# Kernel optimization log

Hardware: AMD Instinct MI355X
Metric: run time of the kernel (lower is better)

The kernel has to match this reference:

```python
import math
import jax, jax.numpy as jnp
import numpy as np

N_HEADS = 16
NUM_BUCKETS = 32
MAX_DISTANCE = 128
ROTARY_BASE = 10000.0


def rotate_half(x):
    x1, x2 = jnp.split(x, 2, axis=-1)
    return jnp.concatenate((-x2, x1), axis=-1)


def rotary_freqs(T, dim):
    inv_freq = 1.0 / (ROTARY_BASE ** (jnp.arange(0, dim, 2, dtype=jnp.float32) / dim))
    t = jnp.arange(T, dtype=jnp.float32)
    freqs = jnp.einsum('i,j->ij', t, inv_freq)  # [T, dim/2]
    return jnp.concatenate((freqs, freqs), axis=-1)  # [T, dim]


def rel_pos_bucket_causal(rel_pos, num_buckets=NUM_BUCKETS, max_distance=MAX_DISTANCE):
    n = jnp.maximum(-rel_pos, 0)  # [T, T] int
    max_exact = num_buckets // 2
    is_small = n < max_exact
    n_safe = jnp.maximum(n, 1).astype(jnp.float32)
    val_if_large = max_exact + (
        jnp.log(n_safe / max_exact) / math.log(max_distance / max_exact) * (num_buckets - max_exact)
    ).astype(jnp.int32)
    val_if_large = jnp.minimum(val_if_large, num_buckets - 1)
    return jnp.where(is_small, n, val_if_large)


def setup_inputs() -> dict:
    key = jax.random.key(0)
    ks = jax.random.split(key, 10)
    B, T, C = 2, 2048, 1024
    s = 0.02
    return {
        'x':  jax.random.normal(ks[0], (B, T, C), dtype=jnp.float32),
        'Wq': jax.random.normal(ks[1], (C, C), dtype=jnp.float32) * s,
        'bq': jnp.zeros((C,), dtype=jnp.float32),
        'Wk': jax.random.normal(ks[2], (C, C), dtype=jnp.float32) * s,
        'bk': jnp.zeros((C,), dtype=jnp.float32),
        'Wv': jax.random.normal(ks[3], (C, C), dtype=jnp.float32) * s,
        'bv': jnp.zeros((C,), dtype=jnp.float32),
        'Wp': jax.random.normal(ks[4], (C, C), dtype=jnp.float32) * s,
        'bp': jnp.zeros((C,), dtype=jnp.float32),
        'rel_bias_table': jax.random.normal(ks[5], (NUM_BUCKETS, N_HEADS), dtype=jnp.float32) * s,
    }


def reference(x, Wq, bq, Wk, bk, Wv, bv, Wp, bp, rel_bias_table):
    B, T, C = x.shape
    H = N_HEADS
    D = C // H

    def heads(y):
        return y.reshape(B, T, H, D).transpose(0, 2, 1, 3)  # [B,H,T,D]

    q = heads(x @ Wq + bq)
    k = heads(x @ Wk + bk)
    v = heads(x @ Wv + bv)

    # rotary (use_xpos=False -> scale=1)
    freqs = rotary_freqs(T, D)  # [T, D]
    cos, sin = jnp.cos(freqs), jnp.sin(freqs)
    q = q * cos + rotate_half(q) * sin
    k = k * cos + rotate_half(k) * sin

    # relative position bias (causal, scale=1.0)
    pos = jnp.arange(T)
    rel_pos = pos[None, :] - pos[:, None]  # k_pos - q_pos
    bucket = rel_pos_bucket_causal(rel_pos)  # [T, T]
    bias = rel_bias_table[bucket]  # [T, T, H]
    bias = bias.transpose(2, 0, 1)  # [H, T, T]

    att = jnp.einsum('bhid,bhjd->bhij', q, k) + bias[None]
    att = att * (1.0 / math.sqrt(D))
    causal = pos[None, :] <= pos[:, None]  # tril mask [T, T]
    att = jnp.where(causal[None, None], att, -jnp.inf)
    att = jax.nn.softmax(att, axis=-1)

    y = jnp.einsum('bhij,bhjd->bhid', att, v)  # [B,H,T,D]
    y = y.transpose(0, 2, 1, 3).reshape(B, T, C)
    return y @ Wp + bp
```

## Files before the change

### kernel.cpp

```cpp
#include <hip/hip_runtime.h>
#include <hip/hip_bf16.h>
#include <math.h>

#define B_ 2
#define T_ 2048
#define C_ 1024
#define H_ 16
#define D_ 64
#define M_ (B_ * T_)
#define K_ 1024

#define SCALE2 0.18033688011112043f

typedef short bf16x8 __attribute__((ext_vector_type(8)));
typedef float f32x4  __attribute__((ext_vector_type(4)));
typedef unsigned int u32;

__device__ __forceinline__ float u2f(unsigned short u) {
    union { unsigned int i; float f; } v; v.i = ((unsigned int)u) << 16; return v.f;
}
__device__ __forceinline__ unsigned short f2b(float f) {
    __hip_bfloat16 h = __float2bfloat16(f);
    return *reinterpret_cast<unsigned short*>(&h);
}
__device__ __forceinline__ u32 pack_bf16_rnd(float a, float b) {
    const u32 au = __float_as_uint(a) + 0x8000u;
    const u32 bu = __float_as_uint(b) + 0x8000u;
    return __builtin_amdgcn_perm(bu, au, 0x07060302u);
}
__device__ __forceinline__ void load_lds16(const void* g, void* l) {
    __builtin_amdgcn_global_load_lds(
        (const __attribute__((address_space(1))) u32*)g,
        (__attribute__((address_space(3))) u32*)l, 16, 0, 0);
}

__global__ __launch_bounds__(256) void prep(
    const float* __restrict__ x,
    const float* __restrict__ W0, const float* __restrict__ W1,
    const float* __restrict__ W2, const float* __restrict__ W3,
    const float* __restrict__ tbl,
    unsigned short* __restrict__ xb,
    unsigned short* __restrict__ T0, unsigned short* __restrict__ T1,
    unsigned short* __restrict__ T2, unsigned short* __restrict__ T3,
    float* __restrict__ dtab, float2* __restrict__ trig)
{
    __shared__ __align__(16) unsigned short tile[64][72];
    const int bx = blockIdx.x;
    const int tid = threadIdx.x;

    if (bx < 2048) {
        const int idx = bx * 256 + tid;
        const float4 a = reinterpret_cast<const float4*>(x)[idx * 2];
        const float4 b = reinterpret_cast<const float4*>(x)[idx * 2 + 1];
        unsigned short t[8] = {f2b(a.x), f2b(a.y), f2b(a.z), f2b(a.w),
                               f2b(b.x), f2b(b.y), f2b(b.z), f2b(b.w)};
        reinterpret_cast<bf16x8*>(xb)[idx] = *reinterpret_cast<const bf16x8*>(t);
    } else if (bx < 3072) {
        const int w = bx - 2048;
        const int z = w >> 8;
        const int rem = w & 255;
        const int k0 = (rem & 15) * 64, n0 = (rem >> 4) * 64;
        const float* W = z == 0 ? W0 : z == 1 ? W1 : z == 2 ? W2 : W3;
        unsigned short* Wt = z == 0 ? T0 : z == 1 ? T1 : z == 2 ? T2 : T3;

        #pragma unroll
        for (int it = 0; it < 4; ++it) {
            const int idx = it * 256 + tid;
            const int r = idx >> 4, c = (idx & 15) * 4;
            const float4 w4 = *reinterpret_cast<const float4*>(W + (size_t)(k0 + r) * C_ + n0 + c);
            tile[r][c + 0] = f2b(w4.x); tile[r][c + 1] = f2b(w4.y);
            tile[r][c + 2] = f2b(w4.z); tile[r][c + 3] = f2b(w4.w);
        }
        __syncthreads();
        #pragma unroll
        for (int it = 0; it < 2; ++it) {
            const int idx = it * 256 + tid;
            const int nc = idx >> 3, kc = (idx & 7) * 8;
            unsigned short tmp[8];
            #pragma unroll
            for (int e = 0; e < 8; ++e) tmp[e] = tile[kc + e][nc];
            *reinterpret_cast<bf16x8*>(Wt + (size_t)(n0 + nc) * K_ + k0 + kc) =
                *reinterpret_cast<const bf16x8*>(tmp);
        }
    } else {
        const int idx = (bx - 3072) * 256 + tid;
        if (idx < H_ * T_) {
            const int h = idx >> 11, n = idx & (T_ - 1);
            int bucket;
            if (n < 16) bucket = n;
            else {
                int vb = 16 + (int)(log2f((float)n * 0.0625f) * (16.0f / 3.0f));
                bucket = vb < 31 ? vb : 31;
            }
            dtab[idx] = tbl[bucket * H_ + h] * SCALE2;
        }
        const int t = idx >> 5, j = idx & 31;
        const float inv = exp2f(-(float)j * (13.287712379549449f / 32.0f));
        const float ang = (float)t * inv;
        trig[idx] = make_float2(cosf(ang), sinf(ang));
    }
}

__device__ __forceinline__ void gemm_core(
    const unsigned short* __restrict__ A, const unsigned short* __restrict__ Bt,
    const float* __restrict__ bias, const float2* __restrict__ trig,
    float rot_scale, float* __restrict__ outf,
    unsigned short* __restrict__ outb, int mode)
{
    __shared__ __align__(16) unsigned short As[128 * 32];
    __shared__ __align__(16) unsigned short Bs[128 * 32];

    const int tid = threadIdx.x;
    const int wid = tid >> 6, lane = tid & 63;
    const int l16 = lane & 15, quad = lane >> 4;
    const int wm = wid >> 1, wn = wid & 1;
    const int m0 = blockIdx.y * 128, n0 = blockIdx.x * 128;

    f32x4 acc[4][4];
    #pragma unroll
    for (int i = 0; i < 4; ++i)
        #pragma unroll
        for (int j = 0; j < 4; ++j) acc[i][j] = (f32x4){0.f, 0.f, 0.f, 0.f};

    char* AsB = (char*)As;
    char* BsB = (char*)Bs;

    for (int k0 = 0; k0 < K_; k0 += 32) {
        __syncthreads();
        #pragma unroll
        for (int it = 0; it < 2; ++it) {
            const int idx = it * 256 + tid;
            const int row = idx >> 2, ch = (idx & 3) * 8;
            const int ldso = it * 4096 + wid * 1024;
            load_lds16(A + (size_t)(m0 + row) * K_ + k0 + ch, AsB + ldso);
            load_lds16(Bt + (size_t)(n0 + row) * K_ + k0 + ch, BsB + ldso);
        }
        __syncthreads();

        bf16x8 af[4], bf[4];
        #pragma unroll
        for (int i = 0; i < 4; ++i) {
            af[i] = *reinterpret_cast<const bf16x8*>(&As[(wm * 64 + i * 16 + l16) * 32 + quad * 8]);
            bf[i] = *reinterpret_cast<const bf16x8*>(&Bs[(wn * 64 + i * 16 + l16) * 32 + quad * 8]);
        }
        #pragma unroll
        for (int i = 0; i < 4; ++i)
            #pragma unroll
            for (int j = 0; j < 4; ++j)
                acc[i][j] = __builtin_amdgcn_mfma_f32_16x16x32_bf16(af[i], bf[j], acc[i][j], 0, 0, 0);
    }

    if (mode == 1) {
        #pragma unroll
        for (int i = 0; i < 4; ++i) {
            const int mb = m0 + wm * 64 + i * 16 + quad * 4;
            const int bb = mb >> 11, tb = mb & (T_ - 1);
            #pragma unroll
            for (int jc = 0; jc < 2; ++jc) {
                const int n_lo = n0 + wn * 64 + jc * 16 + l16;
                const int h = n_lo >> 6, d = n_lo & 63;
                const float bv_lo = bias[n_lo], bv_hi = bias[n_lo + 32];
                unsigned short* po = outb + (((size_t)bb * H_ + h) * T_ + tb) * D_ + d;
                #pragma unroll
                for (int r = 0; r < 4; ++r) {
                    const float2 cs = trig[(tb + r) * 32 + d];
                    const float a = acc[i][jc][r] + bv_lo;
                    const float b = acc[i][jc + 2][r] + bv_hi;
                    po[(size_t)r * D_]      = f2b((a * cs.x - b * cs.y) * rot_scale);
                    po[(size_t)r * D_ + 32] = f2b((b * cs.x + a * cs.y) * rot_scale);
                }
            }
        }
        return;
    }

    #pragma unroll
    for (int i = 0; i < 4; ++i) {
        const int mb = m0 + wm * 64 + i * 16 + quad * 4;
        #pragma unroll
        for (int j = 0; j < 4; ++j) {
            const int n = n0 + wn * 64 + j * 16 + l16;
            const float bv = bias[n];
            if (mode == 2) {
                const int bb = mb >> 11, t = mb & (T_ - 1);
                const int h = n >> 6, d = n & 63;
                uint2 w;
                w.x = pack_bf16_rnd(acc[i][j][0] + bv, acc[i][j][1] + bv);
                w.y = pack_bf16_rnd(acc[i][j][2] + bv, acc[i][j][3] + bv);
                *reinterpret_cast<uint2*>(
                    outb + (((size_t)bb * H_ + h) * D_ + d) * T_ + t) = w;
            } else {
                #pragma unroll
                for (int r = 0; r < 4; ++r)
                    outf[(size_t)(mb + r) * C_ + n] = acc[i][j][r] + bv;
            }
        }
    }
}

__global__ __launch_bounds__(256) void gemm_qkv(
    const unsigned short* __restrict__ A,
    const unsigned short* __restrict__ Wq, const unsigned short* __restrict__ Wk,
    const unsigned short* __restrict__ Wv,
    const float* __restrict__ bq, const float* __restrict__ bk,
    const float* __restrict__ bv, const float2* __restrict__ trig,
    unsigned short* __restrict__ Qo, unsigned short* __restrict__ Ko,
    unsigned short* __restrict__ Vto)
{
    const int z = blockIdx.z;
    const unsigned short* Bt = z == 0 ? Wq : z == 1 ? Wk : Wv;
    const float* bias = z == 0 ? bq : z == 1 ? bk : bv;
    unsigned short* outb = z == 0 ? Qo : z == 1 ? Ko : Vto;
    const float rs = z == 0 ? SCALE2 : 1.0f;
    gemm_core(A, Bt, bias, trig, rs, nullptr, outb, z == 2 ? 2 : 1);
}

__global__ __launch_bounds__(256) void gemm_proj(
    const unsigned short* __restrict__ A, const unsigned short* __restrict__ Bt,
    const float* __restrict__ bias, float* __restrict__ outf)
{
    gemm_core(A, Bt, bias, nullptr, 1.0f, outf, nullptr, 0);
}

__global__ __launch_bounds__(256) void flash_attn(
    const unsigned short* __restrict__ Q, const unsigned short* __restrict__ K,
    const unsigned short* __restrict__ Vt, const float* __restrict__ dtab,
    unsigned short* __restrict__ Y)
{
    __shared__ __align__(16) unsigned short Ks[2][64][72];
    __shared__ __align__(16) unsigned short Vs[2][64][72];
    __shared__ __align__(16) unsigned short Ps[4][16][72];
    __shared__ __align__(16) float bias_ls[64 + T_];

    const int lin = (int)(blockIdx.y * gridDim.x + blockIdx.x);
    const int bh  = lin & 31;
    const int rem = lin >> 5;
    const int h = bh & (H_ - 1), b = bh >> 4;
    const int tid = threadIdx.x;
    const int wid = tid >> 6, lane = tid & 63;
    const int l16 = lane & 15, quad = lane >> 4;
    const size_t base = (size_t)bh * T_ * D_;
    const size_t vbase = (size_t)bh * D_ * T_;

    const int qta = (rem + bh) & 15;
    const int qtb = 31 - qta;

    if (tid < 64) bias_ls[tid] = -INFINITY;
    for (int ii = tid; ii < qtb * 64 + 64; ii += 256) bias_ls[64 + ii] = dtab[h * T_ + ii];

    bf16x8 ones;
    #pragma unroll
    for (int e = 0; e < 8; ++e) ones[e] = (short)0x3F80;

    const int sr0 = tid >> 3,         sch0 = (tid & 7) * 8;
    const int sr1 = (tid + 256) >> 3, sch1 = ((tid + 256) & 7) * 8;

    bf16x8 kr[2], vr[2];
    kr[0] = *reinterpret_cast<const bf16x8*>(K + base + (size_t)sr0 * D_ + sch0);
    kr[1] = *reinterpret_cast<const bf16x8*>(K + base + (size_t)sr1 * D_ + sch1);
    vr[0] = *reinterpret_cast<const bf16x8*>(Vt + vbase + (size_t)sr0 * T_ + sch0);
    vr[1] = *reinterpret_cast<const bf16x8*>(Vt + vbase + (size_t)sr1 * T_ + sch1);
    *reinterpret_cast<bf16x8*>(&Ks[0][sr0][sch0]) = kr[0];
    *reinterpret_cast<bf16x8*>(&Ks[0][sr1][sch1]) = kr[1];
    *reinterpret_cast<bf16x8*>(&Vs[0][sr0][sch0]) = vr[0];
    *reinterpret_cast<bf16x8*>(&Vs[0][sr1][sch1]) = vr[1];
    kr[0] = *reinterpret_cast<const bf16x8*>(K + base + (size_t)(64 + sr0) * D_ + sch0);
    kr[1] = *reinterpret_cast<const bf16x8*>(K + base + (size_t)(64 + sr1) * D_ + sch1);
    vr[0] = *reinterpret_cast<const bf16x8*>(Vt + vbase + (size_t)sr0 * T_ + 64 + sch0);
    vr[1] = *reinterpret_cast<const bf16x8*>(Vt + vbase + (size_t)sr1 * T_ + 64 + sch1);
    __syncthreads();

    int t = 0;
    for (int qi = 0; qi < 2; ++qi) {
        const int qt = qi ? qta : qtb;
        const int q0 = qt * 64;
        const int arow = q0 + wid * 16 + l16;
        const int crow = q0 + wid * 16 + quad * 4;
        const int nbase = crow - l16 * 4;

        bf16x8 qf[2];
        qf[0] = *reinterpret_cast<const bf16x8*>(Q + base + (size_t)arow * D_ + quad * 8);
        qf[1] = *reinterpret_cast<const bf16x8*>(Q + base + (size_t)arow * D_ + 32 + quad * 8);

        f32x4 o[4], ol;
        #pragma unroll
        for (int c = 0; c < 4; ++c) o[c] = (f32x4){0.f, 0.f, 0.f, 0.f};
        ol = (f32x4){0.f, 0.f, 0.f, 0.f};

        for (int kt = 0; kt <= qt; ++kt, ++t) {
            const int j0 = kt * 64;
            const int cur = t & 1, nxt = cur ^ 1;

            if (t < 32) {
                *reinterpret_cast<bf16x8*>(&Ks[nxt][sr0][sch0]) = kr[0];
                *reinterpret_cast<bf16x8*>(&Ks[nxt][sr1][sch1]) = kr[1];
                *reinterpret_cast<bf16x8*>(&Vs[nxt][sr0][sch0]) = vr[0];
                *reinterpret_cast<bf16x8*>(&Vs[nxt][sr1][sch1]) = vr[1];
            }
            if (t < 31) {
                const int tn = t + 2;
                const int jn = (tn <= qtb ? tn : tn - qtb - 1) * 64;
                kr[0] = *reinterpret_cast<const bf16x8*>(K + base + (size_t)(jn + sr0) * D_ + sch0);
                kr[1] = *reinterpret_cast<const bf16x8*>(K + base + (size_t)(jn + sr1) * D_ + sch1);
                vr[0] = *reinterpret_cast<const bf16x8*>(Vt + vbase + (size_t)sr0 * T_ + jn + sch0);
                vr[1] = *reinterpret_cast<const bf16x8*>(Vt + vbase + (size_t)sr1 * T_ + jn + sch1);
            }

            const int d0 = nbase - j0;
            const f32x4 blo = *reinterpret_cast<const f32x4*>(&bias_ls[60 + d0]);
            const f32x4 bhi = *reinterpret_cast<const f32x4*>(&bias_ls[64 + d0]);

            f32x4 sc[4];
            #pragma unroll
            for (int c = 0; c < 4; ++c) {
                #pragma unroll
                for (int r = 0; r < 4; ++r)
                    sc[c][r] = (r >= c) ? bhi[r - c] : blo[4 + r - c];
            }
            __builtin_amdgcn_s_setprio(1);
            #pragma unroll
            for (int c = 0; c < 4; ++c) {
                #pragma unroll
                for (int s = 0; s < 2; ++s) {
                    bf16x8 kf = *reinterpret_cast<const bf16x8*>(
                        &Ks[cur][l16 * 4 + c][s * 32 + quad * 8]);
                    sc[c] = __builtin_amdgcn_mfma_f32_16x16x32_bf16(qf[s], kf, sc[c], 0, 0, 0);
                }
            }
            __builtin_amdgcn_s_setprio(0);

            #pragma unroll
            for (int r = 0; r < 4; ++r) {
                const float p0 = __builtin_amdgcn_exp2f(sc[0][r]);
                const float p1 = __builtin_amdgcn_exp2f(sc[1][r]);
                const float p2 = __builtin_amdgcn_exp2f(sc[2][r]);
                const float p3 = __builtin_amdgcn_exp2f(sc[3][r]);
                uint2 w;
                w.x = pack_bf16_rnd(p0, p1);
                w.y = pack_bf16_rnd(p2, p3);
                *reinterpret_cast<uint2*>(&Ps[wid][quad * 4 + r][l16 * 4]) = w;
            }

            __builtin_amdgcn_s_setprio(1);
            #pragma unroll
            for (int s = 0; s < 2; ++s) {
                bf16x8 pf = *reinterpret_cast<const bf16x8*>(&Ps[wid][l16][s * 32 + quad * 8]);
                #pragma unroll
                for (int c = 0; c < 4; ++c) {
                    bf16x8 vf = *reinterpret_cast<const bf16x8*>(&Vs[cur][c * 16 + l16][s * 32 + quad * 8]);
                    o[c] = __builtin_amdgcn_mfma_f32_16x16x32_bf16(pf, vf, o[c], 0, 0, 0);
                }
                ol = __builtin_amdgcn_mfma_f32_16x16x32_bf16(pf, ones, ol, 0, 0, 0);
            }
            __builtin_amdgcn_s_setprio(0);

            __syncthreads();
        }

        #pragma unroll
        for (int r = 0; r < 4; ++r) {
            const int i = crow + r;
            const float invl = 1.0f / ol[r];
            #pragma unroll
            for (int c = 0; c < 4; ++c)
                Y[((size_t)b * T_ + i) * C_ + h * D_ + c * 16 + l16] = f2b(o[c][r] * invl);
        }
    }
}

extern "C" void kernel_launch(void* const* d_in, const int* in_sizes, int n_in,
                              void* d_out, int out_size, void* d_ws, size_t ws_size,
                              hipStream_t stream)
{
    const float* x   = (const float*)d_in[0];
    const float* Wq  = (const float*)d_in[1];
    const float* bq  = (const float*)d_in[2];
    const float* Wk  = (const float*)d_in[3];
    const float* bk  = (const float*)d_in[4];
    const float* Wv  = (const float*)d_in[5];
    const float* bv  = (const float*)d_in[6];
    const float* Wp  = (const float*)d_in[7];
    const float* bp  = (const float*)d_in[8];
    const float* tbl = (const float*)d_in[9];
    float* out = (float*)d_out;

    const size_t n1 = (size_t)B_ * H_ * T_ * D_;
    const size_t nW = (size_t)C_ * C_;
    unsigned short* xb  = (unsigned short*)d_ws;
    unsigned short* Wqt = xb + (size_t)M_ * K_;
    unsigned short* Wkt = Wqt + nW;
    unsigned short* Wvt = Wkt + nW;
    unsigned short* Wpt = Wvt + nW;
    unsigned short* Qb  = Wpt + nW;
    unsigned short* Kb  = Qb + n1;
    unsigned short* Vtb = Kb + n1;
    unsigned short* Yb  = Vtb + n1;
    float* dtab = (float*)(Yb + n1);
    float2* trig = (float2*)(dtab + H_ * T_);

    const dim3 blk(256);

    prep<<<dim3(3328), blk, 0, stream>>>(x, Wq, Wk, Wv, Wp, tbl,
                                         xb, Wqt, Wkt, Wvt, Wpt, dtab, trig);

    gemm_qkv<<<dim3(C_ / 128, M_ / 128, 3), blk, 0, stream>>>(
        xb, Wqt, Wkt, Wvt, bq, bk, bv, trig, Qb, Kb, Vtb);

    flash_attn<<<dim3(16, B_ * H_), blk, 0, stream>>>(Qb, Kb, Vtb, dtab, Yb);

    gemm_proj<<<dim3(C_ / 128, M_ / 128), blk, 0, stream>>>(Yb, Wpt, bp, out);
}
```

Baseline: 207.4 us.

## Double-buffer GEMM LDS tiles, remap blocks per XCD, shrink proj tile to 128x64

The GEMM main loop now double-buffers LDS, issuing the next k-slice's global-to-LDS loads before the current slice's MFMAs, with one barrier per iteration instead of two. Block indices are remapped so consecutive tiles land on the same XCD (lin&7 grouping), which should improve L2 reuse of A/B panels. The projection GEMM switches to a 128x64 tile, doubling its block count to 512 for better CU occupancy on 256 CUs. LDS use doubles, which may reduce occupancy, and the smaller proj tile lowers arithmetic intensity per block.

After: 211.8 us. +2.1%, slower.

```diff
diff --git a/kernel.cpp b/kernel.cpp
--- a/kernel.cpp
+++ b/kernel.cpp
@@ -101,53 +101,67 @@
     }
 }
 
+template<int BN>
 __device__ __forceinline__ void gemm_core(
     const unsigned short* __restrict__ A, const unsigned short* __restrict__ Bt,
     const float* __restrict__ bias, const float2* __restrict__ trig,
     float rot_scale, float* __restrict__ outf,
-    unsigned short* __restrict__ outb, int mode)
-{
-    __shared__ __align__(16) unsigned short As[128 * 32];
-    __shared__ __align__(16) unsigned short Bs[128 * 32];
+    unsigned short* __restrict__ outb, int mode, int m0, int n0)
+{
+    constexpr int FN  = BN / 32;
+    constexpr int BCH = BN / 64;
+    __shared__ __align__(16) unsigned short As[2][128 * 32];
+    __shared__ __align__(16) unsigned short Bs[2][BN * 32];
 
     const int tid = threadIdx.x;
     const int wid = tid >> 6, lane = tid & 63;
     const int l16 = lane & 15, quad = lane >> 4;
     const int wm = wid >> 1, wn = wid & 1;
-    const int m0 = blockIdx.y * 128, n0 = blockIdx.x * 128;
-
-    f32x4 acc[4][4];
+
+    f32x4 acc[4][FN];
     #pragma unroll
     for (int i = 0; i < 4; ++i)
         #pragma unroll
-        for (int j = 0; j < 4; ++j) acc[i][j] = (f32x4){0.f, 0.f, 0.f, 0.f};
-
-    char* AsB = (char*)As;
-    char* BsB = (char*)Bs;
-
-    for (int k0 = 0; k0 < K_; k0 += 32) {
-        __syncthreads();
+        for (int j = 0; j < FN; ++j) acc[i][j] = (f32x4){0.f, 0.f, 0.f, 0.f};
+
+    auto stage = [&](int buf, int k0) {
         #pragma unroll
         for (int it = 0; it < 2; ++it) {
             const int idx = it * 256 + tid;
             const int row = idx >> 2, ch = (idx & 3) * 8;
-            const int ldso = it * 4096 + wid * 1024;
-            load_lds16(A + (size_t)(m0 + row) * K_ + k0 + ch, AsB + ldso);
-            load_lds16(Bt + (size_t)(n0 + row) * K_ + k0 + ch, BsB + ldso);
-        }
-        __syncthreads();
-
-        bf16x8 af[4], bf[4];
-        #pragma unroll
-        for (int i = 0; i < 4; ++i) {
-            af[i] = *reinterpret_cast<const bf16x8*>(&As[(wm * 64 + i * 16 + l16) * 32 + quad * 8]);
-            bf[i] = *reinterpret_cast<const bf16x8*>(&Bs[(wn * 64 + i * 16 + l16) * 32 + quad * 8]);
-        }
+            load_lds16(A + (size_t)(m0 + row) * K_ + k0 + ch,
+                       (char*)As[buf] + it * 4096 + wid * 1024);
+        }
+        #pragma unroll
+        for (int it = 0; it < BCH; ++it) {
+            const int idx = it * 256 + tid;
+            const int row = idx >> 2, ch = (idx & 3) * 8;
+            load_lds16(Bt + (size_t)(n0 + row) * K_ + k0 + ch,
+                       (char*)Bs[buf] + it * 4096 + wid * 1024);
+        }
+    };
+
+    stage(0, 0);
+    __syncthreads();
+
+    for (int k0 = 0, s = 0; k0 < K_; k0 += 32, ++s) {
+        const int cur = s & 1;
+        if (k0 + 32 < K_) stage(cur ^ 1, k0 + 32);
+
+        bf16x8 af[4], bf[FN];
         #pragma unroll
         for (int i = 0; i < 4; ++i)
-            #pragma unroll
-            for (int j = 0; j < 4; ++j)
+            af[i] = *reinterpret_cast<const bf16x8*>(&As[cur][(wm * 64 + i * 16 + l16) * 32 + quad * 8]);
+        #pragma unroll
+        for (int j = 0; j < FN; ++j)
+            bf[j] = *reinterpret_cast<const bf16x8*>(&Bs[cur][(wn * (BN / 2) + j * 16 + l16) * 32 + quad * 8]);
+        #pragma unroll
+        for (int i = 0; i < 4; ++i)
+            #pragma unroll
+            for (int j = 0; j < FN; ++j)
                 acc[i][j] = __builtin_amdgcn_mfma_f32_16x16x32_bf16(af[i], bf[j], acc[i][j], 0, 0, 0);
+
+        if (k0 + 32 < K_) __syncthreads();
     }
 
     if (mode == 1) {
@@ -156,8 +170,8 @@
             const int mb = m0 + wm * 64 + i * 16 + quad * 4;
             const int bb = mb >> 11, tb = mb & (T_ - 1);
             #pragma unroll
-            for (int jc = 0; jc < 2; ++jc) {
-                const int n_lo = n0 + wn * 64 + jc * 16 + l16;
+            for (int jc = 0; jc < FN / 2; ++jc) {
+                const int n_lo = n0 + wn * (BN / 2) + jc * 16 + l16;
                 const int h = n_lo >> 6, d = n_lo & 63;
                 const float bv_lo = bias[n_lo], bv_hi = bias[n_lo + 32];
                 unsigned short* po = outb + (((size_t)bb * H_ + h) * T_ + tb) * D_ + d;
@@ -165,7 +179,7 @@
                 for (int r = 0; r < 4; ++r) {
                     const float2 cs = trig[(tb + r) * 32 + d];
                     const float a = acc[i][jc][r] + bv_lo;
-                    const float b = acc[i][jc + 2][r] + bv_hi;
+                    const float b = acc[i][jc + FN / 2][r] + bv_hi;
                     po[(size_t)r * D_]      = f2b((a * cs.x - b * cs.y) * rot_scale);
                     po[(size_t)r * D_ + 32] = f2b((b * cs.x + a * cs.y) * rot_scale);
                 }
@@ -178,8 +192,8 @@
     for (int i = 0; i < 4; ++i) {
         const int mb = m0 + wm * 64 + i * 16 + quad * 4;
         #pragma unroll
-        for (int j = 0; j < 4; ++j) {
-            const int n = n0 + wn * 64 + j * 16 + l16;
+        for (int j = 0; j < FN; ++j) {
+            const int n = n0 + wn * (BN / 2) + j * 16 + l16;
             const float bv = bias[n];
             if (mode == 2) {
                 const int bb = mb >> 11, t = mb & (T_ - 1);
@@ -207,19 +221,28 @@
     unsigned short* __restrict__ Qo, unsigned short* __restrict__ Ko,
     unsigned short* __restrict__ Vto)
 {
-    const int z = blockIdx.z;
+    const int lin = (int)blockIdx.x;
+    const int g = lin & 7, slot = lin >> 3;
+    const int w = g * 96 + slot;
+    const int z = w >> 8, rem = w & 255;
+    const int m0 = (rem >> 3) * 128, n0 = (rem & 7) * 128;
+
     const unsigned short* Bt = z == 0 ? Wq : z == 1 ? Wk : Wv;
     const float* bias = z == 0 ? bq : z == 1 ? bk : bv;
     unsigned short* outb = z == 0 ? Qo : z == 1 ? Ko : Vto;
     const float rs = z == 0 ? SCALE2 : 1.0f;
-    gemm_core(A, Bt, bias, trig, rs, nullptr, outb, z == 2 ? 2 : 1);
+    gemm_core<128>(A, Bt, bias, trig, rs, nullptr, outb, z == 2 ? 2 : 1, m0, n0);
 }
 
 __global__ __launch_bounds__(256) void gemm_proj(
     const unsigned short* __restrict__ A, const unsigned short* __restrict__ Bt,
     const float* __restrict__ bias, float* __restrict__ outf)
 {
-    gemm_core(A, Bt, bias, nullptr, 1.0f, outf, nullptr, 0);
+    const int lin = (int)blockIdx.x;
+    const int g = lin & 7, slot = lin >> 3;
+    const int w = g * 64 + slot;
+    const int m0 = (w >> 4) * 128, n0 = (w & 15) * 64;
+    gemm_core<64>(A, Bt, bias, nullptr, 1.0f, outf, nullptr, 0, m0, n0);
 }
 
 __global__ __launch_bounds__(256) void flash_attn(
@@ -403,10 +426,10 @@
     prep<<<dim3(3328), blk, 0, stream>>>(x, Wq, Wk, Wv, Wp, tbl,
                                          xb, Wqt, Wkt, Wvt, Wpt, dtab, trig);
 
-    gemm_qkv<<<dim3(C_ / 128, M_ / 128, 3), blk, 0, stream>>>(
+    gemm_qkv<<<dim3(768), blk, 0, stream>>>(
         xb, Wqt, Wkt, Wvt, bq, bk, bv, trig, Qb, Kb, Vtb);
 
     flash_attn<<<dim3(16, B_ * H_), blk, 0, stream>>>(Qb, Kb, Vtb, dtab, Yb);
 
-    gemm_proj<<<dim3(C_ / 128, M_ / 128), blk, 0, stream>>>(Yb, Wpt, bp, out);
-}
+    gemm_proj<<<dim3(512), blk, 0, stream>>>(Yb, Wpt, bp, out);
+}
```
